# Kernel tuning notes

Measured on AMD Instinct MI355X. Metric: run time of the kernel, lower is better.

The kernel has to match this reference:

```python
import jax, jax.numpy as jnp
import numpy as np

N, K, CIN, HID, COUT, E, MH = 8192, 200, 512, 256, 40, 5, 64
KG = K // E
EPS = 1e-5


def setup_inputs() -> dict:
    key = jax.random.key(0)
    ks = jax.random.split(key, 20)
    inp = {
        "X": jax.random.normal(ks[0], (N, CIN), jnp.float32),
        "La": jax.random.uniform(ks[1], (K,), jnp.float32),
        "U": jax.random.normal(ks[2], (N, K), jnp.float32),
        # 5 EigenExperts, each mlp = Linear(1,64) -> ReLU -> Linear(64,64) -> ReLU -> Linear(64,1)
        "eW1": jax.random.normal(ks[3], (E, MH), jnp.float32) * 0.5,
        "eb1": jax.random.normal(ks[4], (E, MH), jnp.float32) * 0.1,
        "eW2": jax.random.normal(ks[5], (E, MH, MH), jnp.float32) * (1.0 / np.sqrt(MH)),
        "eb2": jax.random.normal(ks[6], (E, MH), jnp.float32) * 0.1,
        "eW3": jax.random.normal(ks[7], (E, MH), jnp.float32) * (1.0 / np.sqrt(MH)),
        "eb3": jax.random.normal(ks[8], (E,), jnp.float32) * 0.1,
        # gate: Linear(5,5) -> ReLU -> Linear(5,5) -> Softmax
        "gW1": jax.random.normal(ks[9], (E, E), jnp.float32) * 0.4,
        "gb1": jax.random.normal(ks[10], (E,), jnp.float32) * 0.1,
        "gW2": jax.random.normal(ks[11], (E, E), jnp.float32) * 0.4,
        "gb2": jax.random.normal(ks[12], (E,), jnp.float32) * 0.1,
        # W: Linear(in_channels, hidden_dim)
        "Ww": jax.random.normal(ks[13], (CIN, HID), jnp.float32) * (1.0 / np.sqrt(CIN)),
        "Wb": jax.random.normal(ks[14], (HID,), jnp.float32) * 0.1,
        # BatchNorm1d(hidden_dim), training-mode batch stats
        "bn_gamma": jnp.ones((HID,), jnp.float32),
        "bn_beta": jnp.zeros((HID,), jnp.float32),
        # MLP: Linear(hidden_dim, out_channels)
        "Mw": jax.random.normal(ks[15], (HID, COUT), jnp.float32) * (1.0 / np.sqrt(HID)),
        "Mb": jax.random.normal(ks[16], (COUT,), jnp.float32) * 0.1,
    }
    return inp


def reference(X, La, U, eW1, eb1, eW2, eb2, eW3, eb3, gW1, gb1, gW2, gb2, Ww, Wb, bn_gamma, bn_beta, Mw, Mb):
    n, k = U.shape
    e = eW1.shape[0]
    kg = k // e
    # group eigenvector columns: U[:, i*kg:(i+1)*kg] for expert i -> [n, e, kg]
    Ue = U.reshape(n, e, kg)
    # EigenExpert tiny MLP applied elementwise over entries of each column, then mean over nodes
    h1 = jax.nn.relu(jnp.einsum('nek,eh->nekh', Ue, eW1) + eb1[None, :, None, :])
    h2 = jax.nn.relu(jnp.einsum('nekh,ehg->nekg', h1, eW2) + eb2[None, :, None, :])
    v = jnp.einsum('nekh,eh->nek', h2, eW3) + eb3[None, :, None]
    V = v.mean(axis=0)                      # [e, kg] importance per eigenvector
    # gate on per-group mean eigenvalue
    stats = La.reshape(e, kg).mean(axis=1)  # [e]
    g = jax.nn.relu(stats @ gW1 + gb1) @ gW2 + gb2
    g = jax.nn.softmax(g, axis=-1)          # [e]
    # sum_i g_i * U_i diag(V_i) U_i^T == (U * s) @ U^T with per-column scale s
    s = (g[:, None] * V).reshape(k)         # [k]
    A = (U * s[None, :]) @ U.T              # [n, n]
    out = A @ X                             # [n, cin]
    hidden = out @ Ww + Wb                  # [n, hid]
    mu = hidden.mean(axis=0)
    var = hidden.var(axis=0)                # biased, as torch BN uses for normalization
    h = (hidden - mu) * jax.lax.rsqrt(var + EPS) * bn_gamma + bn_beta
    h = jax.nn.relu(h)                      # dropout is identity (eval)
    logits = h @ Mw + Mb
    return jax.nn.log_softmax(logits, axis=1), hidden
```

## Files before the change

### kernel.cpp

```cpp
#include <hip/hip_runtime.h>
#include <hip/hip_bf16.h>

#define N_    8192
#define K_    200
#define CIN_  512
#define HID_  256
#define COUT_ 40
#define E_    5
#define MH_   64
#define KG_   40
#define EPS_  1e-5f

#define WS_VSUM  0
#define WS_BNSUM 256
#define WS_T     768
#define WS_S     103168
#define WS_G     103424

typedef __bf16 bf16x8 __attribute__((ext_vector_type(8)));
typedef float  f32x16 __attribute__((ext_vector_type(16)));

__device__ __forceinline__ uint packbf(float a, float b) {
    union { __bf16 h[2]; uint u; } p;
    p.h[0] = (__bf16)a; p.h[1] = (__bf16)b;
    return p.u;
}

union UB { uint4 q; bf16x8 v; };

__global__ __launch_bounds__(256) void k_expert(
    const float* __restrict__ U,
    const float* __restrict__ eW1, const float* __restrict__ eb1,
    const float* __restrict__ eW2, const float* __restrict__ eb2,
    const float* __restrict__ eW3, const float* __restrict__ eb3,
    float* __restrict__ Vsum)
{
    const int e   = blockIdx.x;
    const int tid = threadIdx.x;
    const int w   = tid >> 6;
    const int l   = tid & 63;
    const int lo  = l & 31;
    const int hi  = l >> 5;

    __shared__ float sW1[MH_], sb1[MH_], sb2s[MH_], sW3s[MH_];
    __shared__ float colsum[KG_];

    if (tid < MH_) {
        sW1[tid]  = eW1[e*MH_ + tid];
        sb1[tid]  = eb1[e*MH_ + tid];
        sb2s[tid] = eb2[e*MH_ + tid];
        sW3s[tid] = eW3[e*MH_ + tid];
    }
    if (tid < KG_) colsum[tid] = 0.f;
    const float b3 = eb3[e];

    bf16x8 fa[2][4];
    {
        const float* W2e = eW2 + e*MH_*MH_;
        #pragma unroll
        for (int mt = 0; mt < 2; ++mt) {
            const int grow = mt*32 + lo;
            #pragma unroll
            for (int t = 0; t < 4; ++t) {
                const int k0 = 16*t + 8*hi;
                union { uint u[4]; bf16x8 v; } fb;
                #pragma unroll
                for (int r = 0; r < 4; ++r) {
                    const float x0 = W2e[(k0+2*r  )*MH_ + grow];
                    const float x1 = W2e[(k0+2*r+1)*MH_ + grow];
                    fb.u[r] = packbf(x0, x1);
                }
                fa[mt][t] = fb.v;
            }
        }
    }
    __syncthreads();

    for (int it = 0; it < 4; ++it) {
        const int tile  = (blockIdx.y*16 + it*4 + w);
        const int elem0 = tile * 64;
        const int idx   = elem0 + l;
        const int n     = idx / KG_;
        const int kg    = idx - n*KG_;
        const float u   = U[n*K_ + e*KG_ + kg];

        const float ucol0 = __shfl(u, lo);
        const float ucol1 = __shfl(u, 32 + lo);

        f32x16 acc00 = {0}; f32x16 acc10 = {0};
        f32x16 acc01 = {0}; f32x16 acc11 = {0};
        #pragma unroll
        for (int t = 0; t < 4; ++t) {
            const int k0 = 16*t + 8*hi;
            float2 w1p[4], b1p[4];
            #pragma unroll
            for (int r = 0; r < 4; ++r) {
                w1p[r] = *reinterpret_cast<const float2*>(&sW1[k0 + 2*r]);
                b1p[r] = *reinterpret_cast<const float2*>(&sb1[k0 + 2*r]);
            }
            union { uint u[4]; bf16x8 v; } b0, b1;
            #pragma unroll
            for (int r = 0; r < 4; ++r) {
                const float pa = fmaxf(fmaf(ucol0, w1p[r].x, b1p[r].x), 0.f);
                const float pb = fmaxf(fmaf(ucol0, w1p[r].y, b1p[r].y), 0.f);
                b0.u[r] = packbf(pa, pb);
                const float qa = fmaxf(fmaf(ucol1, w1p[r].x, b1p[r].x), 0.f);
                const float qb = fmaxf(fmaf(ucol1, w1p[r].y, b1p[r].y), 0.f);
                b1.u[r] = packbf(qa, qb);
            }
            acc00 = __builtin_amdgcn_mfma_f32_32x32x16_bf16(fa[0][t], b0.v, acc00, 0, 0, 0);
            acc10 = __builtin_amdgcn_mfma_f32_32x32x16_bf16(fa[1][t], b0.v, acc10, 0, 0, 0);
            acc01 = __builtin_amdgcn_mfma_f32_32x32x16_bf16(fa[0][t], b1.v, acc01, 0, 0, 0);
            acc11 = __builtin_amdgcn_mfma_f32_32x32x16_bf16(fa[1][t], b1.v, acc11, 0, 0, 0);
        }

        float vs0 = 0.f, vs1 = 0.f;
        #pragma unroll
        for (int r = 0; r < 16; ++r) {
            const int gb  = (r & 3) + 8*(r >> 2) + 4*hi;
            const float b2a = sb2s[gb],      w3a = sW3s[gb];
            const float b2b = sb2s[32 + gb], w3b = sW3s[32 + gb];
            vs0 += fmaxf(acc00[r] + b2a, 0.f)*w3a + fmaxf(acc10[r] + b2b, 0.f)*w3b;
            vs1 += fmaxf(acc01[r] + b2a, 0.f)*w3a + fmaxf(acc11[r] + b2b, 0.f)*w3b;
        }
        vs0 += __shfl_xor(vs0, 32);
        vs1 += __shfl_xor(vs1, 32);

        const float myv    = (hi ? vs1 : vs0) + b3;
        const int   myelem = (hi ? 32 : 0) + lo;
        const int   mykg   = (elem0 + myelem) % KG_;
        atomicAdd(&colsum[mykg], myv);
    }

    __syncthreads();
    if (tid < KG_) atomicAdd(&Vsum[e*KG_ + tid], colsum[tid]);
}

__global__ void k_gate(
    const float* __restrict__ La,
    const float* __restrict__ gW1, const float* __restrict__ gb1,
    const float* __restrict__ gW2, const float* __restrict__ gb2,
    const float* __restrict__ Vsum, float* __restrict__ s)
{
    __shared__ float sg[E_];
    const int tid = threadIdx.x;
    if (tid == 0) {
        float stats[E_], g1[E_], g2[E_];
        for (int e = 0; e < E_; ++e) {
            float acc = 0.f;
            for (int k = 0; k < KG_; ++k) acc += La[e*KG_ + k];
            stats[e] = acc * (1.0f/KG_);
        }
        for (int j = 0; j < E_; ++j) {
            float acc = gb1[j];
            for (int i = 0; i < E_; ++i) acc += stats[i]*gW1[i*E_ + j];
            g1[j] = fmaxf(acc, 0.f);
        }
        float m = -1e30f;
        for (int j = 0; j < E_; ++j) {
            float acc = gb2[j];
            for (int i = 0; i < E_; ++i) acc += g1[i]*gW2[i*E_ + j];
            g2[j] = acc;
            m = fmaxf(m, acc);
        }
        float ssum = 0.f;
        for (int j = 0; j < E_; ++j) { g2[j] = expf(g2[j]-m); ssum += g2[j]; }
        for (int j = 0; j < E_; ++j) sg[j] = g2[j] / ssum;
    }
    __syncthreads();
    if (tid < K_) s[tid] = sg[tid / KG_] * Vsum[tid] * (1.0f/N_);
}

__global__ __launch_bounds__(256) void k_utx(
    const float* __restrict__ U, const float* __restrict__ X,
    float* __restrict__ T)
{
    const int c0    = blockIdx.x * 32;
    const int r0    = blockIdx.y * 128;
    const int mhalf = blockIdx.z;
    const int tid = threadIdx.x;
    const int w   = tid >> 6;
    const int l   = tid & 63;
    const int lo  = l & 31;
    const int hi  = l >> 5;

    const int mt   = mhalf*4 + w;
    const int colc = min(32*mt + lo, K_ - 1);
    const int xcol = c0 + lo;

    f32x16 acc = {0};
    #pragma unroll
    for (int s = 0; s < 8; ++s) {
        const int kr = r0 + 16*s + 8*hi;
        union { uint u[4]; bf16x8 v; } ax, bx;
        #pragma unroll
        for (int j2 = 0; j2 < 4; ++j2) {
            const float ua = U[(kr + 2*j2    )*K_ + colc];
            const float ub = U[(kr + 2*j2 + 1)*K_ + colc];
            ax.u[j2] = packbf(ua, ub);
            const float xa = X[(kr + 2*j2    )*CIN_ + xcol];
            const float xb = X[(kr + 2*j2 + 1)*CIN_ + xcol];
            bx.u[j2] = packbf(xa, xb);
        }
        acc = __builtin_amdgcn_mfma_f32_32x32x16_bf16(ax.v, bx.v, acc, 0, 0, 0);
    }

    #pragma unroll
    for (int r = 0; r < 16; ++r) {
        const int mm = 32*mt + (r & 3) + 8*(r >> 2) + 4*hi;
        if (mm < K_)
            atomicAdd(&T[mm*CIN_ + c0 + lo], acc[r]);
    }
}

__global__ __launch_bounds__(256) void k_g(
    const float* __restrict__ T, const float* __restrict__ Ww,
    float* __restrict__ G)
{
    const int k0  = blockIdx.x * 4;
    const int c   = threadIdx.x;
    __shared__ float4 sT4[4][128];

    for (int j = threadIdx.x; j < 512; j += 256) {
        const int r = j >> 7, c4 = j & 127;
        sT4[r][c4] = reinterpret_cast<const float4*>(T)[(k0+r)*128 + c4];
    }
    __syncthreads();

    float a0 = 0.f, a1 = 0.f, a2 = 0.f, a3 = 0.f;
    for (int ci4 = 0; ci4 < 128; ++ci4) {
        const float w0 = Ww[(4*ci4+0)*HID_ + c];
        const float w1 = Ww[(4*ci4+1)*HID_ + c];
        const float w2 = Ww[(4*ci4+2)*HID_ + c];
        const float w3 = Ww[(4*ci4+3)*HID_ + c];
        float4 t;
        t = sT4[0][ci4]; a0 += t.x*w0 + t.y*w1 + t.z*w2 + t.w*w3;
        t = sT4[1][ci4]; a1 += t.x*w0 + t.y*w1 + t.z*w2 + t.w*w3;
        t = sT4[2][ci4]; a2 += t.x*w0 + t.y*w1 + t.z*w2 + t.w*w3;
        t = sT4[3][ci4]; a3 += t.x*w0 + t.y*w1 + t.z*w2 + t.w*w3;
    }
    G[(k0+0)*HID_ + c] = a0;
    G[(k0+1)*HID_ + c] = a1;
    G[(k0+2)*HID_ + c] = a2;
    G[(k0+3)*HID_ + c] = a3;
}

__global__ __launch_bounds__(256) void k_hidden(
    const float* __restrict__ U, const float* __restrict__ s,
    const float* __restrict__ G, const float* __restrict__ Wb,
    float* __restrict__ hid)
{
    const int c0  = blockIdx.x * 64;
    const int n0  = blockIdx.y * 128;
    const int tid = threadIdx.x;
    const int w   = tid >> 6;
    const int l   = tid & 63;
    const int lo  = l & 31;
    const int hi  = l >> 5;

    __shared__ uint  spkA[104][128];
    __shared__ uint  spkB[104][64];
    __shared__ float ss[K_];

    if (tid < K_) ss[tid] = s[tid];
    __syncthreads();

    for (int j = tid; j < 128*26; j += 256) {
        const int m = j & 127, g = j >> 7;
        uint4 pk = make_uint4(0u, 0u, 0u, 0u);
        if (g < 25) {
            const float4 a = *reinterpret_cast<const float4*>(&U[(n0+m)*K_ + 8*g]);
            const float4 b = *reinterpret_cast<const float4*>(&U[(n0+m)*K_ + 8*g + 4]);
            pk.x = packbf(a.x*ss[8*g+0], a.y*ss[8*g+1]);
            pk.y = packbf(a.z*ss[8*g+2], a.w*ss[8*g+3]);
            pk.z = packbf(b.x*ss[8*g+4], b.y*ss[8*g+5]);
            pk.w = packbf(b.z*ss[8*g+6], b.w*ss[8*g+7]);
        }
        spkA[4*g+0][m] = pk.x;
        spkA[4*g+1][m] = pk.y;
        spkA[4*g+2][m] = pk.z;
        spkA[4*g+3][m] = pk.w;
    }
    for (int j = tid; j < 64*26; j += 256) {
        const int c = j & 63, g = j >> 6;
        uint4 pk = make_uint4(0u, 0u, 0u, 0u);
        if (g < 25) {
            const float v0 = G[(8*g+0)*HID_ + c0+c], v1 = G[(8*g+1)*HID_ + c0+c];
            const float v2 = G[(8*g+2)*HID_ + c0+c], v3 = G[(8*g+3)*HID_ + c0+c];
            const float v4 = G[(8*g+4)*HID_ + c0+c], v5 = G[(8*g+5)*HID_ + c0+c];
            const float v6 = G[(8*g+6)*HID_ + c0+c], v7 = G[(8*g+7)*HID_ + c0+c];
            pk.x = packbf(v0, v1); pk.y = packbf(v2, v3);
            pk.z = packbf(v4, v5); pk.w = packbf(v6, v7);
        }
        spkB[4*g+0][c] = pk.x;
        spkB[4*g+1][c] = pk.y;
        spkB[4*g+2][c] = pk.z;
        spkB[4*g+3][c] = pk.w;
    }
    __syncthreads();

    f32x16 acc0 = {0}, acc1 = {0};
    #pragma unroll
    for (int t = 0; t < 13; ++t) {
        const int kp = 8*t + 4*hi;
        union { uint u[4]; bf16x8 v; } fa;
        fa.u[0] = spkA[kp+0][32*w + lo];
        fa.u[1] = spkA[kp+1][32*w + lo];
        fa.u[2] = spkA[kp+2][32*w + lo];
        fa.u[3] = spkA[kp+3][32*w + lo];
        UB b0, b1;
        b0.q.x = spkB[kp+0][lo];      b0.q.y = spkB[kp+1][lo];
        b0.q.z = spkB[kp+2][lo];      b0.q.w = spkB[kp+3][lo];
        b1.q.x = spkB[kp+0][32 + lo]; b1.q.y = spkB[kp+1][32 + lo];
        b1.q.z = spkB[kp+2][32 + lo]; b1.q.w = spkB[kp+3][32 + lo];
        acc0 = __builtin_amdgcn_mfma_f32_32x32x16_bf16(fa.v, b0.v, acc0, 0, 0, 0);
        acc1 = __builtin_amdgcn_mfma_f32_32x32x16_bf16(fa.v, b1.v, acc1, 0, 0, 0);
    }

    const float wb0 = Wb[c0 + lo], wb1 = Wb[c0 + 32 + lo];
    #pragma unroll
    for (int r = 0; r < 16; ++r) {
        const int row = 32*w + (r & 3) + 8*(r >> 2) + 4*hi;
        hid[(n0+row)*HID_ + c0 + lo]      = acc0[r] + wb0;
        hid[(n0+row)*HID_ + c0 + 32 + lo] = acc1[r] + wb1;
    }
}

__global__ __launch_bounds__(256) void k_bnstat(
    const float* __restrict__ hid, float* __restrict__ bnsum)
{
    const int c  = threadIdx.x;
    const int n0 = blockIdx.x * 32;
    float sm = 0.f, sq = 0.f;
    for (int r = 0; r < 32; ++r) {
        const float v = hid[(n0+r)*HID_ + c];
        sm += v; sq += v*v;
    }
    atomicAdd(&bnsum[c], sm);
    atomicAdd(&bnsum[HID_ + c], sq);
}

__global__ __launch_bounds__(256) void k_logits(
    const float* __restrict__ hid, const float* __restrict__ bnsum,
    const float* __restrict__ gamma, const float* __restrict__ beta,
    const float* __restrict__ Mw, const float* __restrict__ Mb,
    float* __restrict__ outls)
{
    __shared__ float sc[HID_], sh[HID_], sMb[COUT_];
    __shared__ float sMw[HID_][COUT_];
    __shared__ float sPart[8][32][41];

    const int tid = threadIdx.x;
    const int r   = tid & 31;
    const int sl  = tid >> 5;

    {
        const float sm = bnsum[tid], sq = bnsum[HID_+tid];
        const float mu  = sm * (1.0f/N_);
        const float var = sq * (1.0f/N_) - mu*mu;
        const float a   = gamma[tid] * rsqrtf(var + EPS_);
        sc[tid] = a;
        sh[tid] = beta[tid] - mu*a;
    }
    for (int j = tid; j < HID_*COUT_/4; j += 256)
        reinterpret_cast<float4*>(&sMw[0][0])[j] = reinterpret_cast<const float4*>(Mw)[j];
    if (tid < COUT_) sMb[tid] = Mb[tid];
    __syncthreads();

    const int n  = blockIdx.x*32 + r;
    const int cb = sl * 32;
    float acc[COUT_];
    #pragma unroll
    for (int j = 0; j < COUT_; ++j) acc[j] = 0.f;

    const float4* hrow = reinterpret_cast<const float4*>(&hid[n*HID_ + cb]);
    #pragma unroll
    for (int c4 = 0; c4 < 8; ++c4) {
        const float4 h4 = hrow[c4];
        const float hv[4] = {h4.x, h4.y, h4.z, h4.w};
        #pragma unroll
        for (int q = 0; q < 4; ++q) {
            const int c = cb + 4*c4 + q;
            const float hn = fmaxf(hv[q]*sc[c] + sh[c], 0.f);
            #pragma unroll
            for (int j0 = 0; j0 < COUT_; j0 += 4) {
                const float4 wv = *reinterpret_cast<const float4*>(&sMw[c][j0]);
                acc[j0+0] += hn*wv.x; acc[j0+1] += hn*wv.y;
                acc[j0+2] += hn*wv.z; acc[j0+3] += hn*wv.w;
            }
        }
    }
    #pragma unroll
    for (int j = 0; j < COUT_; ++j) sPart[sl][r][j] = acc[j];
    __syncthreads();

    if (tid < 32) {
        const int n2 = blockIdx.x*32 + tid;
        float a2[COUT_];
        #pragma unroll
        for (int j = 0; j < COUT_; ++j) {
            float sum = sMb[j];
            #pragma unroll
            for (int s2 = 0; s2 < 8; ++s2) sum += sPart[s2][tid][j];
            a2[j] = sum;
        }
        float m = -1e30f;
        #pragma unroll
        for (int j = 0; j < COUT_; ++j) m = fmaxf(m, a2[j]);
        float ssum = 0.f;
        #pragma unroll
        for (int j = 0; j < COUT_; ++j) ssum += expf(a2[j] - m);
        const float lse = m + logf(ssum);
        #pragma unroll
        for (int j = 0; j < COUT_; ++j)
            outls[n2*COUT_ + j] = a2[j] - lse;
    }
}

extern "C" void kernel_launch(void* const* d_in, const int* in_sizes, int n_in,
                              void* d_out, int out_size, void* d_ws, size_t ws_size,
                              hipStream_t stream)
{
    const float* X        = (const float*)d_in[0];
    const float* La       = (const float*)d_in[1];
    const float* U        = (const float*)d_in[2];
    const float* eW1      = (const float*)d_in[3];
    const float* eb1      = (const float*)d_in[4];
    const float* eW2      = (const float*)d_in[5];
    const float* eb2      = (const float*)d_in[6];
    const float* eW3      = (const float*)d_in[7];
    const float* eb3      = (const float*)d_in[8];
    const float* gW1      = (const float*)d_in[9];
    const float* gb1      = (const float*)d_in[10];
    const float* gW2      = (const float*)d_in[11];
    const float* gb2      = (const float*)d_in[12];
    const float* Ww       = (const float*)d_in[13];
    const float* Wb       = (const float*)d_in[14];
    const float* bn_gamma = (const float*)d_in[15];
    const float* bn_beta  = (const float*)d_in[16];
    const float* Mw       = (const float*)d_in[17];
    const float* Mb       = (const float*)d_in[18];

    float* out   = (float*)d_out;
    float* ws    = (float*)d_ws;
    float* Vsum  = ws + WS_VSUM;
    float* bnsum = ws + WS_BNSUM;
    float* T     = ws + WS_T;
    float* s     = ws + WS_S;
    float* G     = ws + WS_G;

    float* outls = out;
    float* hid   = out + N_*COUT_;

    hipMemsetAsync(ws, 0, (size_t)(WS_T + K_*CIN_) * sizeof(float), stream);

    k_utx   <<<dim3(16, 64, 2), 256, 0, stream>>>(U, X, T);
    k_expert<<<dim3(E_, 320),   256, 0, stream>>>(U, eW1, eb1, eW2, eb2, eW3, eb3, Vsum);
    k_gate  <<<1,   256, 0, stream>>>(La, gW1, gb1, gW2, gb2, Vsum, s);
    k_g     <<<50,  256, 0, stream>>>(T, Ww, G);
    k_hidden<<<dim3(4, 64), 256, 0, stream>>>(U, s, G, Wb, hid);
    k_bnstat<<<256, 256, 0, stream>>>(hid, bnsum);
    k_logits<<<256, 256, 0, stream>>>(hid, bnsum, bn_gamma, bn_beta, Mw, Mb, outls);
}
```

Baseline: 235.8 us.

## Restructure U^T X kernel with double-buffered loads and fuse BN stats into hidden GEMM

The U^T·X kernel now has each block cover both M halves (two accumulators) over 256 rows. It double-buffers global loads in registers so the next step's loads overlap the current MFMA, and the X loads are reused across the two M tiles. The grid shrinks from 2048 to 512 blocks, which also cuts the number of atomics into T. Separately, the BatchNorm sum and sum-of-squares are now accumulated in the k_hidden epilogue with a cross-half shuffle and atomics, which removes the k_bnstat kernel and its re-read of hid. The cost is more register pressure and fewer blocks in k_utx, plus more atomic contention per bnsum column.

```diff
diff --git a/kernel.cpp b/kernel.cpp
--- a/kernel.cpp
+++ b/kernel.cpp
@@ -171,45 +171,62 @@
     if (tid < K_) s[tid] = sg[tid / KG_] * Vsum[tid] * (1.0f/N_);
 }
 
+#define UTX_LOADS(u0v, u1v, xv, step) {                                      \
+    const int kr_ = r0 + 16*(step) + 8*hi;                                   \
+    _Pragma("unroll") for (int j_ = 0; j_ < 8; ++j_) {                       \
+        u0v[j_] = U[(kr_ + j_)*K_  + col0];                                  \
+        u1v[j_] = U[(kr_ + j_)*K_  + col1];                                  \
+        xv[j_]  = X[(kr_ + j_)*CIN_ + xcol];                                 \
+    } }
+
+#define UTX_CONSUME(u0v, u1v, xv) {                                          \
+    union { uint u[4]; bf16x8 v; } a0_, a1_, b_;                             \
+    _Pragma("unroll") for (int r_ = 0; r_ < 4; ++r_) {                       \
+        a0_.u[r_] = packbf(u0v[2*r_], u0v[2*r_+1]);                          \
+        a1_.u[r_] = packbf(u1v[2*r_], u1v[2*r_+1]);                          \
+        b_.u[r_]  = packbf(xv[2*r_],  xv[2*r_+1]);                           \
+    }                                                                        \
+    acc0 = __builtin_amdgcn_mfma_f32_32x32x16_bf16(a0_.v, b_.v, acc0, 0,0,0);\
+    acc1 = __builtin_amdgcn_mfma_f32_32x32x16_bf16(a1_.v, b_.v, acc1, 0,0,0); }
+
 __global__ __launch_bounds__(256) void k_utx(
     const float* __restrict__ U, const float* __restrict__ X,
     float* __restrict__ T)
 {
-    const int c0    = blockIdx.x * 32;
-    const int r0    = blockIdx.y * 128;
-    const int mhalf = blockIdx.z;
+    const int c0  = blockIdx.x * 32;
+    const int r0  = blockIdx.y * 256;
     const int tid = threadIdx.x;
     const int w   = tid >> 6;
     const int l   = tid & 63;
     const int lo  = l & 31;
     const int hi  = l >> 5;
 
-    const int mt   = mhalf*4 + w;
-    const int colc = min(32*mt + lo, K_ - 1);
+    const int mt0  = w;
+    const int mt1  = 4 + w;
+    const int col0 = 32*mt0 + lo;
+    const int col1 = min(32*mt1 + lo, K_ - 1);
     const int xcol = c0 + lo;
 
-    f32x16 acc = {0};
-    #pragma unroll
-    for (int s = 0; s < 8; ++s) {
-        const int kr = r0 + 16*s + 8*hi;
-        union { uint u[4]; bf16x8 v; } ax, bx;
-        #pragma unroll
-        for (int j2 = 0; j2 < 4; ++j2) {
-            const float ua = U[(kr + 2*j2    )*K_ + colc];
-            const float ub = U[(kr + 2*j2 + 1)*K_ + colc];
-            ax.u[j2] = packbf(ua, ub);
-            const float xa = X[(kr + 2*j2    )*CIN_ + xcol];
-            const float xb = X[(kr + 2*j2 + 1)*CIN_ + xcol];
-            bx.u[j2] = packbf(xa, xb);
-        }
-        acc = __builtin_amdgcn_mfma_f32_32x32x16_bf16(ax.v, bx.v, acc, 0, 0, 0);
+    f32x16 acc0 = {0}, acc1 = {0};
+
+    float Au0[8], Au1[8], Ax[8], Bu0[8], Bu1[8], Bx[8];
+    UTX_LOADS(Au0, Au1, Ax, 0);
+    #pragma unroll
+    for (int s = 0; s < 16; s += 2) {
+        if (s + 1 < 16) UTX_LOADS(Bu0, Bu1, Bx, s + 1);
+        UTX_CONSUME(Au0, Au1, Ax);
+        if (s + 2 < 16) UTX_LOADS(Au0, Au1, Ax, s + 2);
+        if (s + 1 < 16) UTX_CONSUME(Bu0, Bu1, Bx);
     }
 
     #pragma unroll
     for (int r = 0; r < 16; ++r) {
-        const int mm = 32*mt + (r & 3) + 8*(r >> 2) + 4*hi;
-        if (mm < K_)
-            atomicAdd(&T[mm*CIN_ + c0 + lo], acc[r]);
+        const int rr  = (r & 3) + 8*(r >> 2) + 4*hi;
+        const int mm0 = 32*mt0 + rr;
+        atomicAdd(&T[mm0*CIN_ + c0 + lo], acc0[r]);
+        const int mm1 = 32*mt1 + rr;
+        if (mm1 < K_)
+            atomicAdd(&T[mm1*CIN_ + c0 + lo], acc1[r]);
     }
 }
 
@@ -248,7 +265,7 @@
 __global__ __launch_bounds__(256) void k_hidden(
     const float* __restrict__ U, const float* __restrict__ s,
     const float* __restrict__ G, const float* __restrict__ Wb,
-    float* __restrict__ hid)
+    float* __restrict__ hid, float* __restrict__ bnsum)
 {
     const int c0  = blockIdx.x * 64;
     const int n0  = blockIdx.y * 128;
@@ -318,26 +335,25 @@
     }
 
     const float wb0 = Wb[c0 + lo], wb1 = Wb[c0 + 32 + lo];
+    float sm0 = 0.f, sq0 = 0.f, sm1 = 0.f, sq1 = 0.f;
     #pragma unroll
     for (int r = 0; r < 16; ++r) {
         const int row = 32*w + (r & 3) + 8*(r >> 2) + 4*hi;
-        hid[(n0+row)*HID_ + c0 + lo]      = acc0[r] + wb0;
-        hid[(n0+row)*HID_ + c0 + 32 + lo] = acc1[r] + wb1;
-    }
-}
-
-__global__ __launch_bounds__(256) void k_bnstat(
-    const float* __restrict__ hid, float* __restrict__ bnsum)
-{
-    const int c  = threadIdx.x;
-    const int n0 = blockIdx.x * 32;
-    float sm = 0.f, sq = 0.f;
-    for (int r = 0; r < 32; ++r) {
-        const float v = hid[(n0+r)*HID_ + c];
-        sm += v; sq += v*v;
-    }
-    atomicAdd(&bnsum[c], sm);
-    atomicAdd(&bnsum[HID_ + c], sq);
+        const float h0 = acc0[r] + wb0;
+        const float h1 = acc1[r] + wb1;
+        hid[(n0+row)*HID_ + c0 + lo]      = h0;
+        hid[(n0+row)*HID_ + c0 + 32 + lo] = h1;
+        sm0 += h0; sq0 += h0*h0;
+        sm1 += h1; sq1 += h1*h1;
+    }
+    sm0 += __shfl_xor(sm0, 32); sq0 += __shfl_xor(sq0, 32);
+    sm1 += __shfl_xor(sm1, 32); sq1 += __shfl_xor(sq1, 32);
+    if (hi == 0) {
+        atomicAdd(&bnsum[c0 + lo],              sm0);
+        atomicAdd(&bnsum[HID_ + c0 + lo],       sq0);
+        atomicAdd(&bnsum[c0 + 32 + lo],         sm1);
+        atomicAdd(&bnsum[HID_ + c0 + 32 + lo],  sq1);
+    }
 }
 
 __global__ __launch_bounds__(256) void k_logits(
@@ -454,11 +470,10 @@
 
     hipMemsetAsync(ws, 0, (size_t)(WS_T + K_*CIN_) * sizeof(float), stream);
 
-    k_utx   <<<dim3(16, 64, 2), 256, 0, stream>>>(U, X, T);
-    k_expert<<<dim3(E_, 320),   256, 0, stream>>>(U, eW1, eb1, eW2, eb2, eW3, eb3, Vsum);
+    k_utx   <<<dim3(16, 32), 256, 0, stream>>>(U, X, T);
+    k_expert<<<dim3(E_, 320), 256, 0, stream>>>(U, eW1, eb1, eW2, eb2, eW3, eb3, Vsum);
     k_gate  <<<1,   256, 0, stream>>>(La, gW1, gb1, gW2, gb2, Vsum, s);
     k_g     <<<50,  256, 0, stream>>>(T, Ww, G);
-    k_hidden<<<dim3(4, 64), 256, 0, stream>>>(U, s, G, Wb, hid);
-    k_bnstat<<<256, 256, 0, stream>>>(hid, bnsum);
+    k_hidden<<<dim3(4, 64), 256, 0, stream>>>(U, s, G, Wb, hid, bnsum);
     k_logits<<<256, 256, 0, stream>>>(hid, bnsum, bn_gamma, bn_beta, Mw, Mb, outls);
 }
```

Result: faster. 214.6 us (-9.0%).
